# Kernel tuning notes

Hardware: AMD Instinct MI355X
Metric: run time of the kernel (lower is better)

## Reference

```python
import jax, jax.numpy as jnp
import numpy as np

H, F, E_SHARED, E_ROUTED, K = 1024, 4096, 1, 8, 2


def setup_inputs() -> dict:
    key = jax.random.key(0)
    ks = jax.random.split(key, 6)
    x = jax.random.normal(ks[0], (4, 2048, H), dtype=jnp.float32)
    s = 0.02
    shared_up = jax.random.normal(ks[1], (E_SHARED, H, F), dtype=jnp.float32) * s
    shared_down = jax.random.normal(ks[2], (E_SHARED, F, H), dtype=jnp.float32) * s
    routed_up = jax.random.normal(ks[3], (E_ROUTED, H, F), dtype=jnp.float32) * s
    routed_down = jax.random.normal(ks[4], (E_ROUTED, F, H), dtype=jnp.float32) * s
    router_w = jax.random.normal(ks[5], (H, E_ROUTED), dtype=jnp.float32) * s
    return {"x": x, "shared_up": shared_up, "shared_down": shared_down,
            "routed_up": routed_up, "routed_down": routed_down, "router_w": router_w}


def _expert(x, w_up, w_down):
    # ExpertBlock: down(gelu(up(x))), exact (erf) gelu as in torch F.gelu default
    h = jax.nn.gelu(jnp.einsum('bsh,hf->bsf', x, w_up), approximate=False)
    return jnp.einsum('bsf,fh->bsh', h, w_down)


def reference(x, shared_up, shared_down, routed_up, routed_down, router_w):
    # shared experts (always active)
    shared_out = jnp.zeros_like(x)
    for i in range(E_SHARED):
        shared_out = shared_out + _expert(x, shared_up[i], shared_down[i])

    # router: softmax over routed experts, then top-k gating
    probs = jax.nn.softmax(jnp.einsum('bsh,he->bse', x, router_w), axis=-1)
    top_k_prob, top_k_idx = jax.lax.top_k(probs, K)  # [B,S,K]
    # per-expert gate = sum of top-k probs assigned to that expert
    onehot = jax.nn.one_hot(top_k_idx, E_ROUTED, dtype=x.dtype)  # [B,S,K,E]
    gates = jnp.einsum('bsk,bske->bse', top_k_prob, onehot)      # [B,S,E]

    routed_out = jnp.zeros_like(x)
    for e in range(E_ROUTED):  # fixed small loop over experts
        y = _expert(x, routed_up[e], routed_down[e])
        routed_out = routed_out + gates[..., e:e + 1] * y

    return shared_out + routed_out + x
```

## Files before the change

kernel.cpp:

```cpp
#include <hip/hip_runtime.h>
#include <cstdint>
#include <cstddef>

#define HD 1024
#define FF 4096
#define TOK 8192
#define NSEG 9
#define ROWS_ROUTED (TOK*2)
#define ROWS_TOT (ROWS_ROUTED + TOK)

typedef __bf16 bf16;
typedef __bf16 bf16x8 __attribute__((ext_vector_type(8)));
typedef __bf16 bf16x4 __attribute__((ext_vector_type(4)));
typedef float  f32x4  __attribute__((ext_vector_type(4)));

__device__ __forceinline__ void stage16(const void* g, void* l) {
  __builtin_amdgcn_global_load_lds((const __attribute__((address_space(1))) void*)g,
                                   (__attribute__((address_space(3))) void*)l,
                                   16, 0, 0);
}

__device__ __forceinline__ unsigned short bf_bits(float v) {
  bf16 b = (bf16)v;
  return __builtin_bit_cast(unsigned short, b);
}

__device__ __forceinline__ int xcd_remap(int d) {
  return (((d >> 6) << 3) + (d & 7)) * 8 + ((d >> 3) & 7);
}

__global__ void k_init_meta(int* meta) {
  int t = threadIdx.x;
  if (t < 64) meta[t] = 0;
}

__global__ void k_tcvt(const float* __restrict__ routed_up, const float* __restrict__ shared_up,
                       const float* __restrict__ routed_dn, const float* __restrict__ shared_dn,
                       bf16* __restrict__ wupT, bf16* __restrict__ wdnT) {
  int z = blockIdx.z;
  bool isup = z < 9;
  int e = isup ? z : z - 9;
  const float* src = isup ? ((e < 8) ? (routed_up + (size_t)e*HD*FF) : shared_up)
                          : ((e < 8) ? (routed_dn + (size_t)e*FF*HD) : shared_dn);
  bf16* d = (isup ? wupT : wdnT) + (size_t)e*FF*HD;
  int R = isup ? HD : FF, C = isup ? FF : HD;
  int r0 = (isup ? blockIdx.y : blockIdx.x) * 64;
  int c0 = (isup ? blockIdx.x : blockIdx.y) * 64;
  __shared__ float lds[64][65];
  int t = threadIdx.x;
  int tr = t>>4, tc4 = (t&15)*4;
  #pragma unroll
  for (int i=0;i<4;i++) {
    float4 v = *reinterpret_cast<const float4*>(src + (size_t)(r0+tr+i*16)*C + c0 + tc4);
    lds[tr+i*16][tc4+0]=v.x; lds[tr+i*16][tc4+1]=v.y;
    lds[tr+i*16][tc4+2]=v.z; lds[tr+i*16][tc4+3]=v.w;
  }
  __syncthreads();
  #pragma unroll
  for (int i=0;i<4;i++) {
    int oc = tr + i*16;
    ushort4 u;
    u.x = bf_bits(lds[tc4+0][oc]);
    u.y = bf_bits(lds[tc4+1][oc]);
    u.z = bf_bits(lds[tc4+2][oc]);
    u.w = bf_bits(lds[tc4+3][oc]);
    *reinterpret_cast<ushort4*>(d + (size_t)(c0+oc)*R + r0 + tc4) = u;
  }
}

__global__ void k_router(const float* __restrict__ x, const float* __restrict__ rw,
                         bf16* __restrict__ xbf,
                         int* __restrict__ rtE, float* __restrict__ rtG,
                         int* __restrict__ meta) {
  __shared__ float rwl[HD*8];
  int t = threadIdx.x;
  for (int i=t;i<HD*8/4;i+=256)
    reinterpret_cast<float4*>(rwl)[i] = reinterpret_cast<const float4*>(rw)[i];
  __syncthreads();
  int wv = t>>6, lane = t&63;
  int tk = blockIdx.x*4 + wv;
  const float* xr = x + (size_t)tk*HD;
  bf16* xb = xbf + (size_t)tk*HD;
  float a[8] = {0,0,0,0,0,0,0,0};
  for (int i=0;i<HD/64;i++) {
    int h = lane + i*64;
    float xv = xr[h];
    xb[h] = (bf16)xv;
    const float* r = rwl + h*8;
    #pragma unroll
    for (int e=0;e<8;e++) a[e] = fmaf(xv, r[e], a[e]);
  }
  #pragma unroll
  for (int e=0;e<8;e++) {
    for (int s=32;s>0;s>>=1) a[e] += __shfl_xor(a[e], s, 64);
  }
  if (lane==0) {
    float mx = a[0];
    #pragma unroll
    for (int e=1;e<8;e++) mx = fmaxf(mx, a[e]);
    float p[8]; float den = 0.f;
    #pragma unroll
    for (int e=0;e<8;e++) { p[e] = expf(a[e]-mx); den += p[e]; }
    int i0 = 0;
    #pragma unroll
    for (int e=1;e<8;e++) if (p[e] > p[i0]) i0 = e;
    int i1 = (i0==0)?1:0;
    #pragma unroll
    for (int e=0;e<8;e++) if (e!=i0 && p[e] > p[i1]) i1 = e;
    float inv = 1.f/den;
    rtE[tk*2] = i0; rtE[tk*2+1] = i1;
    rtG[tk*2] = p[i0]*inv; rtG[tk*2+1] = p[i1]*inv;
    atomicAdd(&meta[i0], 1);
    atomicAdd(&meta[i1], 1);
  }
}

__global__ void k_prefix(int* meta) {
  if (threadIdx.x == 0) {
    int off = 0;
    for (int e=0;e<8;e++) { meta[16+e] = off; meta[32+e] = meta[e]; off += meta[e]; }
    meta[16+8] = ROWS_ROUTED;
    meta[32+8] = TOK;
  }
}

__global__ void k_scatter(const int* __restrict__ rtE, const float* __restrict__ rtG,
                          int* __restrict__ meta, int* __restrict__ tok,
                          float* __restrict__ gate, int* __restrict__ trow) {
  int t = blockIdx.x*256 + threadIdx.x;
  int e0 = rtE[t*2], e1 = rtE[t*2+1];
  float g0 = rtG[t*2], g1 = rtG[t*2+1];
  int p0 = atomicAdd(&meta[8+e0], 1);
  int r0 = meta[16+e0] + p0;
  tok[r0] = t; gate[r0] = g0; trow[t*2] = r0;
  int p1 = atomicAdd(&meta[8+e1], 1);
  int r1 = meta[16+e1] + p1;
  tok[r1] = t; gate[r1] = g1; trow[t*2+1] = r1;
  tok[ROWS_ROUTED + t] = t; gate[ROWS_ROUTED + t] = 1.0f;
}

__global__ void k_combine(const float* __restrict__ x, const bf16* __restrict__ dbuf,
                          const int* __restrict__ trow, float* __restrict__ out) {
  int tkn = blockIdx.x;
  int t = threadIdx.x;
  int r0 = trow[tkn*2], r1 = trow[tkn*2+1];
  int h = t*4;
  float4 xv = *reinterpret_cast<const float4*>(x + (size_t)tkn*HD + h);
  bf16x4 a = *reinterpret_cast<const bf16x4*>(dbuf + (size_t)(ROWS_ROUTED+tkn)*HD + h);
  bf16x4 b = *reinterpret_cast<const bf16x4*>(dbuf + (size_t)r0*HD + h);
  bf16x4 c = *reinterpret_cast<const bf16x4*>(dbuf + (size_t)r1*HD + h);
  float4 o;
  o.x = xv.x + (float)a[0] + (float)b[0] + (float)c[0];
  o.y = xv.y + (float)a[1] + (float)b[1] + (float)c[1];
  o.z = xv.z + (float)a[2] + (float)b[2] + (float)c[2];
  o.w = xv.w + (float)a[3] + (float)b[3] + (float)c[3];
  *reinterpret_cast<float4*>(out + (size_t)tkn*HD + h) = o;
}


__global__ __launch_bounds__(256,4) void k_gemm_up(
    const bf16* __restrict__ xbf, const bf16* __restrict__ wupT,
    bf16* __restrict__ hbuf, const int* __restrict__ tok,
    const int* __restrict__ meta)
{
  int bx = xcd_remap(blockIdx.x);
  int seg = bx >> 11;
  int rem = bx & 2047;
  int mt = rem >> 5, nt = rem & 31;
  int rows = (seg<8)? meta[32+seg] : TOK;
  if (mt*128 >= rows) return;
  int segoff = meta[16+seg];
  int rowbase = mt*128;

  __shared__ __align__(16) bf16 Alds[2][128*32];
  __shared__ __align__(16) bf16 Blds[2][128*32];

  const int t = threadIdx.x;
  const int lane = t & 63, w = t >> 6;

  int lr0 = t>>2, lr1 = 64 + (t>>2);
  int gr0 = rowbase + lr0; if (gr0 >= rows) gr0 = rowbase;
  int gr1 = rowbase + lr1; if (gr1 >= rows) gr1 = rowbase;
  int tok0 = tok[segoff + gr0], tok1 = tok[segoff + gr1];
  int kswz = ((t&3) ^ ((t>>3)&3)) * 8;
  const bf16* gA0 = xbf + (size_t)tok0*HD + kswz;
  const bf16* gA1 = xbf + (size_t)tok1*HD + kswz;
  const bf16* wb = wupT + (size_t)seg*FF*HD;
  int f0 = nt*128;
  const bf16* gB0 = wb + (size_t)(f0 + lr0)*HD + kswz;
  const bf16* gB1 = wb + (size_t)(f0 + lr1)*HD + kswz;

  char* AldsB = (char*)Alds; char* BldsB = (char*)Blds;
  const int stoff = w*1024;

  const int slotb = ((lane>>4) ^ (((lane&15)>>1)&3)) * 16;
  const int Afo = ((w>>1)*64 + (lane&15))*64 + slotb;
  const int Bfo = ((w&1)*64 + (lane&15))*64 + slotb;

  f32x4 acc[4][4] = {};

  stage16(gA0, AldsB + stoff);
  stage16(gA1, AldsB + 4096 + stoff);
  stage16(gB0, BldsB + stoff);
  stage16(gB1, BldsB + 4096 + stoff);
  __syncthreads();

  int cur = 0;
  for (int k0=32; k0<HD; k0+=32) {
    char* an = AldsB + (cur^1)*8192;
    char* bn = BldsB + (cur^1)*8192;
    stage16(gA0 + k0, an + stoff);
    stage16(gA1 + k0, an + 4096 + stoff);
    stage16(gB0 + k0, bn + stoff);
    stage16(gB1 + k0, bn + 4096 + stoff);
    const char* Ab = AldsB + cur*8192 + Afo;
    const char* Bb = BldsB + cur*8192 + Bfo;
    bf16x8 af[4], bfr[4];
    #pragma unroll
    for (int m=0;m<4;m++) af[m]  = *reinterpret_cast<const bf16x8*>(Ab + m*1024);
    #pragma unroll
    for (int n=0;n<4;n++) bfr[n] = *reinterpret_cast<const bf16x8*>(Bb + n*1024);
    #pragma unroll
    for (int m=0;m<4;m++)
      #pragma unroll
      for (int n=0;n<4;n++)
        acc[m][n] = __builtin_amdgcn_mfma_f32_16x16x32_bf16(bfr[n], af[m], acc[m][n], 0,0,0);
    __syncthreads();
    cur ^= 1;
  }
  {
    const char* Ab = AldsB + cur*8192 + Afo;
    const char* Bb = BldsB + cur*8192 + Bfo;
    bf16x8 af[4], bfr[4];
    #pragma unroll
    for (int m=0;m<4;m++) af[m]  = *reinterpret_cast<const bf16x8*>(Ab + m*1024);
    #pragma unroll
    for (int n=0;n<4;n++) bfr[n] = *reinterpret_cast<const bf16x8*>(Bb + n*1024);
    #pragma unroll
    for (int m=0;m<4;m++)
      #pragma unroll
      for (int n=0;n<4;n++)
        acc[m][n] = __builtin_amdgcn_mfma_f32_16x16x32_bf16(bfr[n], af[m], acc[m][n], 0,0,0);
  }

  const int lrm = lane&15, lq = lane>>4;
  #pragma unroll
  for (int m=0;m<4;m++) {
    int rl = (w>>1)*64 + m*16 + lrm;
    int gr = rowbase + rl;
    if (gr >= rows) continue;
    bf16* hrow = hbuf + (size_t)(segoff+gr)*FF + nt*128 + (w&1)*64 + lq*4;
    #pragma unroll
    for (int n=0;n<4;n++) {
      bf16x4 u;
      #pragma unroll
      for (int j=0;j<4;j++) {
        float v = acc[m][n][j];
        v = 0.5f*v*(1.0f + erff(v*0.70710678118654752f));
        u[j] = (bf16)v;
      }
      *reinterpret_cast<bf16x4*>(hrow + n*16) = u;
    }
  }
}

__global__ __launch_bounds__(256,4) void k_gemm_down(
    const bf16* __restrict__ hbuf, const bf16* __restrict__ wdnT,
    bf16* __restrict__ dbuf, const float* __restrict__ gate,
    const int* __restrict__ meta)
{
  int bx = xcd_remap(blockIdx.x);
  int seg = bx >> 9;
  int rem = bx & 511;
  int mt = rem >> 3, nt = rem & 7;
  int rows = (seg<8)? meta[32+seg] : TOK;
  if (mt*128 >= rows) return;
  int segoff = meta[16+seg];
  int rowbase = mt*128;

  __shared__ __align__(16) bf16 Alds[2][128*32];
  __shared__ __align__(16) bf16 Blds[2][128*32];
  __shared__ float gateL[128];

  const int t = threadIdx.x;
  const int lane = t & 63, w = t >> 6;

  if (t < 128) {
    int gr = rowbase + t; if (gr >= rows) gr = rows - 1;
    gateL[t] = gate[segoff + gr];
  }

  int lr0 = t>>2, lr1 = 64 + (t>>2);
  int kswz = ((t&3) ^ ((t>>3)&3)) * 8;
  const bf16* gA0 = hbuf + (size_t)(segoff + rowbase + lr0)*FF + kswz;
  const bf16* gA1 = hbuf + (size_t)(segoff + rowbase + lr1)*FF + kswz;
  const bf16* wb = wdnT + (size_t)seg*HD*FF;
  int h0 = nt*128;
  const bf16* gB0 = wb + (size_t)(h0 + lr0)*FF + kswz;
  const bf16* gB1 = wb + (size_t)(h0 + lr1)*FF + kswz;

  char* AldsB = (char*)Alds; char* BldsB = (char*)Blds;
  const int stoff = w*1024;

  const int slotb = ((lane>>4) ^ (((lane&15)>>1)&3)) * 16;
  const int Afo = ((w>>1)*64 + (lane&15))*64 + slotb;
  const int Bfo = ((w&1)*64 + (lane&15))*64 + slotb;

  f32x4 acc[4][4] = {};

  stage16(gA0, AldsB + stoff);
  stage16(gA1, AldsB + 4096 + stoff);
  stage16(gB0, BldsB + stoff);
  stage16(gB1, BldsB + 4096 + stoff);
  __syncthreads();

  int cur = 0;
  for (int k0=32; k0<FF; k0+=32) {
    char* an = AldsB + (cur^1)*8192;
    char* bn = BldsB + (cur^1)*8192;
    stage16(gA0 + k0, an + stoff);
    stage16(gA1 + k0, an + 4096 + stoff);
    stage16(gB0 + k0, bn + stoff);
    stage16(gB1 + k0, bn + 4096 + stoff);
    const char* Ab = AldsB + cur*8192 + Afo;
    const char* Bb = BldsB + cur*8192 + Bfo;
    bf16x8 af[4], bfr[4];
    #pragma unroll
    for (int m=0;m<4;m++) af[m]  = *reinterpret_cast<const bf16x8*>(Ab + m*1024);
    #pragma unroll
    for (int n=0;n<4;n++) bfr[n] = *reinterpret_cast<const bf16x8*>(Bb + n*1024);
    #pragma unroll
    for (int m=0;m<4;m++)
      #pragma unroll
      for (int n=0;n<4;n++)
        acc[m][n] = __builtin_amdgcn_mfma_f32_16x16x32_bf16(bfr[n], af[m], acc[m][n], 0,0,0);
    __syncthreads();
    cur ^= 1;
  }
  {
    const char* Ab = AldsB + cur*8192 + Afo;
    const char* Bb = BldsB + cur*8192 + Bfo;
    bf16x8 af[4], bfr[4];
    #pragma unroll
    for (int m=0;m<4;m++) af[m]  = *reinterpret_cast<const bf16x8*>(Ab + m*1024);
    #pragma unroll
    for (int n=0;n<4;n++) bfr[n] = *reinterpret_cast<const bf16x8*>(Bb + n*1024);
    #pragma unroll
    for (int m=0;m<4;m++)
      #pragma unroll
      for (int n=0;n<4;n++)
        acc[m][n] = __builtin_amdgcn_mfma_f32_16x16x32_bf16(bfr[n], af[m], acc[m][n], 0,0,0);
  }

  const int lrm = lane&15, lq = lane>>4;
  #pragma unroll
  for (int m=0;m<4;m++) {
    int rl = (w>>1)*64 + m*16 + lrm;
    int gr = rowbase + rl;
    if (gr >= rows) continue;
    float g = gateL[rl];
    bf16* drow = dbuf + (size_t)(segoff+gr)*HD + nt*128 + (w&1)*64 + lq*4;
    #pragma unroll
    for (int n=0;n<4;n++) {
      bf16x4 u;
      #pragma unroll
      for (int j=0;j<4;j++) u[j] = (bf16)(acc[m][n][j]*g);
      *reinterpret_cast<bf16x4*>(drow + n*16) = u;
    }
  }
}

struct Layout {
  size_t xbf, wupT, wdnT, hbuf, dbuf, tok, gate, trow, rtE, rtG, meta, total;
};

static inline Layout make_layout() {
  Layout L; size_t o = 0;
  auto al = [&](size_t b){ o = (o+255)&~(size_t)255; size_t r=o; o+=b; return r; };
  L.xbf  = al((size_t)TOK*HD*2);
  L.wupT = al((size_t)NSEG*FF*HD*2);
  L.wdnT = al((size_t)NSEG*FF*HD*2);
  L.hbuf = al((size_t)ROWS_TOT*FF*2);
  L.dbuf = al((size_t)ROWS_TOT*HD*2);
  L.tok  = al((size_t)ROWS_TOT*4);
  L.gate = al((size_t)ROWS_TOT*4);
  L.trow = al((size_t)TOK*2*4);
  L.rtE  = al((size_t)TOK*2*4);
  L.rtG  = al((size_t)TOK*2*4);
  L.meta = al(256*4);
  L.total = o;
  return L;
}

extern "C" void kernel_launch(void* const* d_in, const int* in_sizes, int n_in,
                              void* d_out, int out_size, void* d_ws, size_t ws_size,
                              hipStream_t stream) {
  const float* x           = (const float*)d_in[0];
  const float* shared_up   = (const float*)d_in[1];
  const float* shared_down = (const float*)d_in[2];
  const float* routed_up   = (const float*)d_in[3];
  const float* routed_down = (const float*)d_in[4];
  const float* router_w    = (const float*)d_in[5];
  float* out = (float*)d_out;

  Layout L = make_layout();
  char* ws = (char*)d_ws;
  bf16*  xbf  = (bf16*)(ws + L.xbf);
  bf16*  wupT = (bf16*)(ws + L.wupT);
  bf16*  wdnT = (bf16*)(ws + L.wdnT);
  bf16*  hbuf = (bf16*)(ws + L.hbuf);
  bf16*  dbuf = (bf16*)(ws + L.dbuf);
  int*   tok  = (int*)(ws + L.tok);
  float* gate = (float*)(ws + L.gate);
  int*   trow = (int*)(ws + L.trow);
  int*   rtE  = (int*)(ws + L.rtE);
  float* rtG  = (float*)(ws + L.rtG);
  int*   meta = (int*)(ws + L.meta);

  k_init_meta<<<1, 64, 0, stream>>>(meta);
  k_tcvt<<<dim3(64, 16, 18), 256, 0, stream>>>(routed_up, shared_up, routed_down, shared_down, wupT, wdnT);
  k_router<<<TOK/4, 256, 0, stream>>>(x, router_w, xbf, rtE, rtG, meta);
  k_prefix<<<1, 64, 0, stream>>>(meta);
  k_scatter<<<TOK/256, 256, 0, stream>>>(rtE, rtG, meta, tok, gate, trow);

  k_gemm_up<<<NSEG*64*32, 256, 0, stream>>>(xbf, wupT, hbuf, tok, meta);
  k_gemm_down<<<NSEG*64*8, 256, 0, stream>>>(hbuf, wdnT, dbuf, gate, meta);
  k_combine<<<TOK, 256, 0, stream>>>(x, dbuf, trow, out);
}
```

Measured before the change: 999.4 us.

## Deepen GEMM LDS pipeline to four stages with explicit vmcnt waits

Both expert GEMM kernels move from a double-buffered LDS scheme with a full __syncthreads per K-step to a 4-slot ring. Three tiles are prefetched ahead, and the code uses explicit s_waitcnt vmcnt counts plus a bare s_barrier, so loads stay in flight across iterations. The goal is to hide global-load latency better. In exchange, LDS per block grows to 64KB and launch bounds drop from 4 to 2 blocks per CU, which lowers occupancy.

```diff
diff --git a/kernel.cpp b/kernel.cpp
--- a/kernel.cpp
+++ b/kernel.cpp
@@ -158,7 +158,10 @@
 }
 
 
-__global__ __launch_bounds__(256,4) void k_gemm_up(
+#define NKU (HD/32)
+#define NKD (FF/32)
+
+__global__ __launch_bounds__(256,2) void k_gemm_up(
     const bf16* __restrict__ xbf, const bf16* __restrict__ wupT,
     bf16* __restrict__ hbuf, const int* __restrict__ tok,
     const int* __restrict__ meta)
@@ -172,8 +175,7 @@
   int segoff = meta[16+seg];
   int rowbase = mt*128;
 
-  __shared__ __align__(16) bf16 Alds[2][128*32];
-  __shared__ __align__(16) bf16 Blds[2][128*32];
+  __shared__ __align__(16) char lds[4*16384];
 
   const int t = threadIdx.x;
   const int lane = t & 63, w = t >> 6;
@@ -190,57 +192,46 @@
   const bf16* gB0 = wb + (size_t)(f0 + lr0)*HD + kswz;
   const bf16* gB1 = wb + (size_t)(f0 + lr1)*HD + kswz;
 
-  char* AldsB = (char*)Alds; char* BldsB = (char*)Blds;
-  const int stoff = w*1024;
+  const int stA0 = w*1024, stA1 = 4096 + w*1024;
+  const int stB0 = 8192 + w*1024, stB1 = 12288 + w*1024;
 
   const int slotb = ((lane>>4) ^ (((lane&15)>>1)&3)) * 16;
   const int Afo = ((w>>1)*64 + (lane&15))*64 + slotb;
-  const int Bfo = ((w&1)*64 + (lane&15))*64 + slotb;
+  const int Bfo = 8192 + ((w&1)*64 + (lane&15))*64 + slotb;
 
   f32x4 acc[4][4] = {};
 
-  stage16(gA0, AldsB + stoff);
-  stage16(gA1, AldsB + 4096 + stoff);
-  stage16(gB0, BldsB + stoff);
-  stage16(gB1, BldsB + 4096 + stoff);
-  __syncthreads();
-
-  int cur = 0;
-  for (int k0=32; k0<HD; k0+=32) {
-    char* an = AldsB + (cur^1)*8192;
-    char* bn = BldsB + (cur^1)*8192;
-    stage16(gA0 + k0, an + stoff);
-    stage16(gA1 + k0, an + 4096 + stoff);
-    stage16(gB0 + k0, bn + stoff);
-    stage16(gB1 + k0, bn + 4096 + stoff);
-    const char* Ab = AldsB + cur*8192 + Afo;
-    const char* Bb = BldsB + cur*8192 + Bfo;
+  #pragma unroll
+  for (int k=0;k<3;k++) {
+    char* b = lds + k*16384; int ko = k*32;
+    stage16(gA0+ko, b+stA0); stage16(gA1+ko, b+stA1);
+    stage16(gB0+ko, b+stB0); stage16(gB1+ko, b+stB1);
+  }
+  asm volatile("s_waitcnt vmcnt(8)" ::: "memory");
+  __builtin_amdgcn_s_barrier();
+
+  for (int kt = 0; kt < NKU; ++kt) {
+    if (kt + 3 < NKU) {
+      char* nb = lds + ((kt+3)&3)*16384;
+      int ko = (kt+3)*32;
+      stage16(gA0+ko, nb+stA0); stage16(gA1+ko, nb+stA1);
+      stage16(gB0+ko, nb+stB0); stage16(gB1+ko, nb+stB1);
+    }
+    const char* cb = lds + (kt&3)*16384;
     bf16x8 af[4], bfr[4];
     #pragma unroll
-    for (int m=0;m<4;m++) af[m]  = *reinterpret_cast<const bf16x8*>(Ab + m*1024);
-    #pragma unroll
-    for (int n=0;n<4;n++) bfr[n] = *reinterpret_cast<const bf16x8*>(Bb + n*1024);
+    for (int m=0;m<4;m++) af[m]  = *reinterpret_cast<const bf16x8*>(cb + Afo + m*1024);
+    #pragma unroll
+    for (int n=0;n<4;n++) bfr[n] = *reinterpret_cast<const bf16x8*>(cb + Bfo + n*1024);
     #pragma unroll
     for (int m=0;m<4;m++)
       #pragma unroll
       for (int n=0;n<4;n++)
         acc[m][n] = __builtin_amdgcn_mfma_f32_16x16x32_bf16(bfr[n], af[m], acc[m][n], 0,0,0);
-    __syncthreads();
-    cur ^= 1;
-  }
-  {
-    const char* Ab = AldsB + cur*8192 + Afo;
-    const char* Bb = BldsB + cur*8192 + Bfo;
-    bf16x8 af[4], bfr[4];
-    #pragma unroll
-    for (int m=0;m<4;m++) af[m]  = *reinterpret_cast<const bf16x8*>(Ab + m*1024);
-    #pragma unroll
-    for (int n=0;n<4;n++) bfr[n] = *reinterpret_cast<const bf16x8*>(Bb + n*1024);
-    #pragma unroll
-    for (int m=0;m<4;m++)
-      #pragma unroll
-      for (int n=0;n<4;n++)
-        acc[m][n] = __builtin_amdgcn_mfma_f32_16x16x32_bf16(bfr[n], af[m], acc[m][n], 0,0,0);
+    if (kt + 3 < NKU)      asm volatile("s_waitcnt vmcnt(8)" ::: "memory");
+    else if (kt + 2 < NKU) asm volatile("s_waitcnt vmcnt(4)" ::: "memory");
+    else if (kt + 1 < NKU) asm volatile("s_waitcnt vmcnt(0)" ::: "memory");
+    if (kt + 1 < NKU) __builtin_amdgcn_s_barrier();
   }
 
   const int lrm = lane&15, lq = lane>>4;
@@ -264,7 +255,7 @@
   }
 }
 
-__global__ __launch_bounds__(256,4) void k_gemm_down(
+__global__ __launch_bounds__(256,2) void k_gemm_down(
     const bf16* __restrict__ hbuf, const bf16* __restrict__ wdnT,
     bf16* __restrict__ dbuf, const float* __restrict__ gate,
     const int* __restrict__ meta)
@@ -278,8 +269,7 @@
   int segoff = meta[16+seg];
   int rowbase = mt*128;
 
-  __shared__ __align__(16) bf16 Alds[2][128*32];
-  __shared__ __align__(16) bf16 Blds[2][128*32];
+  __shared__ __align__(16) char lds[4*16384];
   __shared__ float gateL[128];
 
   const int t = threadIdx.x;
@@ -299,57 +289,46 @@
   const bf16* gB0 = wb + (size_t)(h0 + lr0)*FF + kswz;
   const bf16* gB1 = wb + (size_t)(h0 + lr1)*FF + kswz;
 
-  char* AldsB = (char*)Alds; char* BldsB = (char*)Blds;
-  const int stoff = w*1024;
+  const int stA0 = w*1024, stA1 = 4096 + w*1024;
+  const int stB0 = 8192 + w*1024, stB1 = 12288 + w*1024;
 
   const int slotb = ((lane>>4) ^ (((lane&15)>>1)&3)) * 16;
   const int Afo = ((w>>1)*64 + (lane&15))*64 + slotb;
-  const int Bfo = ((w&1)*64 + (lane&15))*64 + slotb;
+  const int Bfo = 8192 + ((w&1)*64 + (lane&15))*64 + slotb;
 
   f32x4 acc[4][4] = {};
 
-  stage16(gA0, AldsB + stoff);
-  stage16(gA1, AldsB + 4096 + stoff);
-  stage16(gB0, BldsB + stoff);
-  stage16(gB1, BldsB + 4096 + stoff);
-  __syncthreads();
-
-  int cur = 0;
-  for (int k0=32; k0<FF; k0+=32) {
-    char* an = AldsB + (cur^1)*8192;
-    char* bn = BldsB + (cur^1)*8192;
-    stage16(gA0 + k0, an + stoff);
-    stage16(gA1 + k0, an + 4096 + stoff);
-    stage16(gB0 + k0, bn + stoff);
-    stage16(gB1 + k0, bn + 4096 + stoff);
-    const char* Ab = AldsB + cur*8192 + Afo;
-    const char* Bb = BldsB + cur*8192 + Bfo;
+  #pragma unroll
+  for (int k=0;k<3;k++) {
+    char* b = lds + k*16384; int ko = k*32;
+    stage16(gA0+ko, b+stA0); stage16(gA1+ko, b+stA1);
+    stage16(gB0+ko, b+stB0); stage16(gB1+ko, b+stB1);
+  }
+  asm volatile("s_waitcnt vmcnt(8)" ::: "memory");
+  __builtin_amdgcn_s_barrier();
+
+  for (int kt = 0; kt < NKD; ++kt) {
+    if (kt + 3 < NKD) {
+      char* nb = lds + ((kt+3)&3)*16384;
+      int ko = (kt+3)*32;
+      stage16(gA0+ko, nb+stA0); stage16(gA1+ko, nb+stA1);
+      stage16(gB0+ko, nb+stB0); stage16(gB1+ko, nb+stB1);
+    }
+    const char* cb = lds + (kt&3)*16384;
     bf16x8 af[4], bfr[4];
     #pragma unroll
-    for (int m=0;m<4;m++) af[m]  = *reinterpret_cast<const bf16x8*>(Ab + m*1024);
-    #pragma unroll
-    for (int n=0;n<4;n++) bfr[n] = *reinterpret_cast<const bf16x8*>(Bb + n*1024);
+    for (int m=0;m<4;m++) af[m]  = *reinterpret_cast<const bf16x8*>(cb + Afo + m*1024);
+    #pragma unroll
+    for (int n=0;n<4;n++) bfr[n] = *reinterpret_cast<const bf16x8*>(cb + Bfo + n*1024);
     #pragma unroll
     for (int m=0;m<4;m++)
       #pragma unroll
       for (int n=0;n<4;n++)
         acc[m][n] = __builtin_amdgcn_mfma_f32_16x16x32_bf16(bfr[n], af[m], acc[m][n], 0,0,0);
-    __syncthreads();
-    cur ^= 1;
-  }
-  {
-    const char* Ab = AldsB + cur*8192 + Afo;
-    const char* Bb = BldsB + cur*8192 + Bfo;
-    bf16x8 af[4], bfr[4];
-    #pragma unroll
-    for (int m=0;m<4;m++) af[m]  = *reinterpret_cast<const bf16x8*>(Ab + m*1024);
-    #pragma unroll
-    for (int n=0;n<4;n++) bfr[n] = *reinterpret_cast<const bf16x8*>(Bb + n*1024);
-    #pragma unroll
-    for (int m=0;m<4;m++)
-      #pragma unroll
-      for (int n=0;n<4;n++)
-        acc[m][n] = __builtin_amdgcn_mfma_f32_16x16x32_bf16(bfr[n], af[m], acc[m][n], 0,0,0);
+    if (kt + 3 < NKD)      asm volatile("s_waitcnt vmcnt(8)" ::: "memory");
+    else if (kt + 2 < NKD) asm volatile("s_waitcnt vmcnt(4)" ::: "memory");
+    else if (kt + 1 < NKD) asm volatile("s_waitcnt vmcnt(0)" ::: "memory");
+    if (kt + 1 < NKD) __builtin_amdgcn_s_barrier();
   }
 
   const int lrm = lane&15, lq = lane>>4;
```

Result: slower. 1.115 ms (+11.6%).
